# Performance work log

Measured on AMD Instinct MI355X. Metric: run time of the kernel, lower is better.

The kernel has to match this reference:

```python
import jax, jax.numpy as jnp
import numpy as np

COMMITMENT_COST = 0.25


def setup_inputs() -> dict:
    key = jax.random.key(0)
    k1, k2 = jax.random.split(key, 2)
    inputs = jax.random.normal(k1, (8, 2048, 1024), dtype=jnp.float32)
    # per-head codebooks: [H=4, K=1024, dh=256]
    codebook = jax.random.normal(k2, (4, 1024, 256), dtype=jnp.float32)
    return {"inputs": inputs, "codebook": codebook}


def reference(inputs, codebook):
    H, K, dh = codebook.shape
    flat = inputs.reshape(-1, H, dh)  # [N, H, dh]
    # squared-euclidean distances per head: [H, N, K]
    x_sq = jnp.sum(flat * flat, axis=-1).T[:, :, None]          # [H, N, 1]
    c_sq = jnp.sum(codebook * codebook, axis=-1)[:, None, :]    # [H, 1, K]
    dots = jnp.einsum('nhd,hkd->hnk', flat, codebook)           # [H, N, K]
    distances = x_sq + c_sq - 2.0 * dots
    idx = jnp.argmin(distances, axis=-1)                        # [H, N]
    # gather codebook rows (equivalent to one-hot @ codebook)
    q = jnp.take_along_axis(codebook, idx[:, :, None], axis=1)  # [H, N, dh]
    quantized = jnp.transpose(q, (1, 0, 2)).reshape(inputs.shape)
    # ema=True, eval mode: q_latent_loss = 0
    e_latent_loss = jnp.mean((jax.lax.stop_gradient(quantized) - inputs) ** 2)
    loss = COMMITMENT_COST * e_latent_loss
    # residual=False: straight-through estimator
    quantized_out = inputs + jax.lax.stop_gradient(quantized - inputs)
    return loss, quantized_out
```

## Files before the change

kernel.cpp:

```cpp
#include <hip/hip_runtime.h>
#include <cfloat>

#define NH    4
#define NK    1024
#define DHD   256
#define NTOK  16384
#define ROWS  (NH * DHD)

typedef __attribute__((ext_vector_type(8))) short bf16x8;
typedef __attribute__((ext_vector_type(4))) float f32x4;

#define WS_CSQ  ((size_t)0)
#define WS_BH   ((size_t)16384)
#define WS_BL   (WS_BH + (size_t)2097152)
#define WS_NEED (WS_BL + (size_t)2097152)

__device__ __forceinline__ unsigned short f32_to_bf16_rn(float f) {
    unsigned u = __float_as_uint(f);
    u += 0x7FFFu + ((u >> 16) & 1u);
    return (unsigned short)(u >> 16);
}
__device__ __forceinline__ float bf16_as_f32(unsigned short h) {
    return __uint_as_float(((unsigned)h) << 16);
}

__device__ __forceinline__ void gload_lds16(const uint4* g, uint4* l) {
    __builtin_amdgcn_global_load_lds(
        (const __attribute__((address_space(1))) void*)g,
        (__attribute__((address_space(3))) void*)l, 16, 0, 0);
}

__global__ __launch_bounds__(64) void csq_kernel(const float* __restrict__ cb,
                                                 float* __restrict__ csq) {
    const int code = blockIdx.x;
    const int lane = threadIdx.x;
    const float4 v = *(const float4*)(cb + (size_t)code * DHD + lane * 4);
    float s = v.x * v.x + v.y * v.y + v.z * v.z + v.w * v.w;
#pragma unroll
    for (int off = 32; off > 0; off >>= 1) s += __shfl_down(s, off, 64);
    if (lane == 0) csq[code] = s;
}

__global__ __launch_bounds__(256) void cvt_cb_kernel(const float* __restrict__ cb,
                                                     uint4* __restrict__ bch,
                                                     uint4* __restrict__ bcl) {
    const int g = blockIdx.x * 8 + (threadIdx.x >> 5);
    const int o = threadIdx.x & 31;
    const float* src = cb + (size_t)g * DHD + o * 8;
    unsigned wh[4], wl[4];
#pragma unroll
    for (int i = 0; i < 4; ++i) {
        const float f0 = src[2 * i], f1 = src[2 * i + 1];
        const unsigned short h0 = f32_to_bf16_rn(f0);
        const unsigned short h1 = f32_to_bf16_rn(f1);
        const unsigned short l0 = f32_to_bf16_rn(f0 - bf16_as_f32(h0));
        const unsigned short l1 = f32_to_bf16_rn(f1 - bf16_as_f32(h1));
        wh[i] = (unsigned)h0 | ((unsigned)h1 << 16);
        wl[i] = (unsigned)l0 | ((unsigned)l1 << 16);
    }
    const int hh = g >> 10, c = g & 1023, dc = o >> 2, kk = o & 3;
    const size_t unit = (size_t)((hh * 8 + dc) * 4 + kk) * NK + c;
    bch[unit] = make_uint4(wh[0], wh[1], wh[2], wh[3]);
    bcl[unit] = make_uint4(wl[0], wl[1], wl[2], wl[3]);
}

__device__ __forceinline__ bool lt_vi(float v, int i, float w, int j) {
    return (v < w) || (v == w && i < j);
}

__device__ __forceinline__ float np_sq_pairwise256(const float* __restrict__ a) {
#pragma clang fp contract(off)
    float tot = 0.f;
#pragma unroll
    for (int blk = 0; blk < 2; ++blk) {
        const float* p = a + blk * 128;
        float r0 = p[0] * p[0], r1 = p[1] * p[1], r2 = p[2] * p[2], r3 = p[3] * p[3];
        float r4 = p[4] * p[4], r5 = p[5] * p[5], r6 = p[6] * p[6], r7 = p[7] * p[7];
#pragma clang loop unroll_count(2)
        for (int i = 8; i < 128; i += 8) {
            r0 = r0 + p[i + 0] * p[i + 0];
            r1 = r1 + p[i + 1] * p[i + 1];
            r2 = r2 + p[i + 2] * p[i + 2];
            r3 = r3 + p[i + 3] * p[i + 3];
            r4 = r4 + p[i + 4] * p[i + 4];
            r5 = r5 + p[i + 5] * p[i + 5];
            r6 = r6 + p[i + 6] * p[i + 6];
            r7 = r7 + p[i + 7] * p[i + 7];
        }
        const float res = ((r0 + r1) + (r2 + r3)) + ((r4 + r5) + (r6 + r7));
        tot = (blk == 0) ? res : (tot + res);
    }
    return tot;
}

__device__ __forceinline__ float np_dot_seq256(const float* __restrict__ a,
                                               const float* __restrict__ b) {
#pragma clang fp contract(off)
    float s = 0.f;
#pragma clang loop unroll_count(4)
    for (int i = 0; i < 256; ++i) s = s + a[i] * b[i];
    return s;
}

__global__ __launch_bounds__(256, 2) void vq_mfma(const float* __restrict__ x,
                                                  const float* __restrict__ cb,
                                                  const float* __restrict__ csq,
                                                  const uint4* __restrict__ bch,
                                                  const uint4* __restrict__ bcl,
                                                  float* __restrict__ out) {
    __shared__ uint4 BsH[2048];
    __shared__ uint4 BsL[2048];
    __shared__ float Cs[NK];
    __shared__ int   Cand[128][2];
    __shared__ int   SIdx[128];
    __shared__ float WSum[4];

    const int tid  = threadIdx.x;
    const int h    = blockIdx.y;
    const int t0   = blockIdx.x * 128;
    const int wv   = tid >> 6;
    const int lane = tid & 63;
    const int kk   = lane >> 4;
    const int ln   = lane & 15;

    const float* xh  = x  + (size_t)t0 * ROWS + h * DHD;
    const float* cbh = cb + (size_t)h * NK * DHD;

#pragma unroll
    for (int i = tid; i < NK; i += 256) Cs[i] = csq[h * NK + i];

    bf16x8 aH[2][8], aL[2][8];
    {
        const int tokb = t0 + wv * 32 + ln;
        const float* xa = x + (size_t)tokb * ROWS + h * DHD + kk * 8;
#pragma unroll
        for (int rt = 0; rt < 2; ++rt) {
#pragma unroll
            for (int dc = 0; dc < 8; ++dc) {
                const float* p = xa + (size_t)(rt * 16) * ROWS + dc * 32;
                const float4 f0 = *(const float4*)p;
                const float4 f1 = *(const float4*)(p + 4);
                const float f[8] = {f0.x, f0.y, f0.z, f0.w, f1.x, f1.y, f1.z, f1.w};
                bf16x8 hv, lv;
#pragma unroll
                for (int j = 0; j < 8; ++j) {
                    const unsigned short hb = f32_to_bf16_rn(f[j]);
                    hv[j] = (short)hb;
                    lv[j] = (short)f32_to_bf16_rn(f[j] - bf16_as_f32(hb));
                }
                aH[rt][dc] = hv;
                aL[rt][dc] = lv;
            }
        }
    }

    float b1[8], b2[8];
    int   i1[8], i2[8];
#pragma unroll
    for (int s = 0; s < 8; ++s) { b1[s] = FLT_MAX; b2[s] = FLT_MAX; i1[s] = 0; i2[s] = 0; }

    for (int k0 = 0; k0 < NK; k0 += 64) {
        __syncthreads();
#pragma unroll
        for (int p = 0; p < 8; ++p) {
            const size_t w = (size_t)(h * 32 + p * 4 + wv) * NK + k0 + lane;
            gload_lds16(&bch[w], &BsH[p * 256 + wv * 64]);
            gload_lds16(&bcl[w], &BsL[p * 256 + wv * 64]);
        }
        __syncthreads();

        f32x4 acc[2][4];
#pragma unroll
        for (int rt = 0; rt < 2; ++rt)
#pragma unroll
            for (int ct = 0; ct < 4; ++ct) acc[rt][ct] = (f32x4){0.f, 0.f, 0.f, 0.f};

#pragma unroll
        for (int dc = 0; dc < 8; ++dc) {
#pragma unroll
            for (int ct = 0; ct < 4; ++ct) {
                const int bu = (dc * 4 + kk) * 64 + ct * 16 + ln;
                const bf16x8 bH = *(const bf16x8*)&BsH[bu];
                const bf16x8 bL = *(const bf16x8*)&BsL[bu];
#pragma unroll
                for (int rt = 0; rt < 2; ++rt) {
                    acc[rt][ct] = __builtin_amdgcn_mfma_f32_16x16x32_bf16(aH[rt][dc], bH, acc[rt][ct], 0, 0, 0);
                    acc[rt][ct] = __builtin_amdgcn_mfma_f32_16x16x32_bf16(aH[rt][dc], bL, acc[rt][ct], 0, 0, 0);
                    acc[rt][ct] = __builtin_amdgcn_mfma_f32_16x16x32_bf16(aL[rt][dc], bH, acc[rt][ct], 0, 0, 0);
                }
            }
        }

#pragma unroll
        for (int rt = 0; rt < 2; ++rt)
#pragma unroll
            for (int ct = 0; ct < 4; ++ct) {
                const float cs   = Cs[k0 + ct * 16 + ln];
                const int   codg = k0 + ct * 16 + ln;
#pragma unroll
                for (int r = 0; r < 4; ++r) {
                    const float dist = cs - 2.f * acc[rt][ct][r];
                    const int   s    = rt * 4 + r;
                    if (dist < b1[s]) { b2[s] = b1[s]; i2[s] = i1[s]; b1[s] = dist; i1[s] = codg; }
                    else if (dist < b2[s]) { b2[s] = dist; i2[s] = codg; }
                }
            }
    }

#pragma unroll
    for (int s = 0; s < 8; ++s) {
        float v1 = b1[s], v2 = b2[s];
        int   j1 = i1[s], j2 = i2[s];
#pragma unroll
        for (int m = 1; m <= 8; m <<= 1) {
            const float o1 = __shfl_xor(v1, m, 64);
            const int   oj1 = __shfl_xor(j1, m, 64);
            const float o2 = __shfl_xor(v2, m, 64);
            const int   oj2 = __shfl_xor(j2, m, 64);
            if (lt_vi(o1, oj1, v1, j1)) {
                if (lt_vi(v1, j1, o2, oj2)) { v2 = v1; j2 = j1; }
                else                        { v2 = o2; j2 = oj2; }
                v1 = o1; j1 = oj1;
            } else if (lt_vi(o1, oj1, v2, j2)) {
                v2 = o1; j2 = oj1;
            }
        }
        if (ln == 0) {
            const int tl = wv * 32 + (s >> 2) * 16 + kk * 4 + (s & 3);
            Cand[tl][0] = j1;
            Cand[tl][1] = j2;
        }
    }
    __syncthreads();

    {
        const int token = tid >> 1;
        const int cand  = tid & 1;
        const int code  = Cand[token][cand];
        const float* xr = xh + (size_t)token * ROWS;
        const float* cr = cbh + (size_t)code * DHD;
        const float X = np_sq_pairwise256(xr);
        const float C = np_sq_pairwise256(cr);
        const float D = np_dot_seq256(xr, cr);
        float d;
        {
#pragma clang fp contract(off)
            const float t = X + C;
            d = t - 2.0f * D;
        }
        const float od = __shfl_xor(d, 1, 64);
        if (cand == 0) {
            const int jA = code;
            const int jB = Cand[token][1];
            const bool pickB = (od < d) || (od == d && jB < jA);
            SIdx[token] = pickB ? jB : jA;
        }
    }
    __syncthreads();

    float lacc = 0.f;
    for (int t = wv; t < 128; t += 4) {
        const float4 q4 = *(const float4*)(cbh + (size_t)SIdx[t] * DHD + (lane << 2));
        const float4 x4 = *(const float4*)(xh + (size_t)t * ROWS + (lane << 2));
        const float dx = q4.x - x4.x, dy = q4.y - x4.y;
        const float dz = q4.z - x4.z, dw = q4.w - x4.w;
        lacc += dx * dx + dy * dy + dz * dz + dw * dw;
        *(float4*)(out + 1 + (size_t)(t0 + t) * ROWS + h * DHD + (lane << 2)) = q4;
    }
#pragma unroll
    for (int off = 32; off > 0; off >>= 1) lacc += __shfl_down(lacc, off, 64);
    if (lane == 0) WSum[wv] = lacc;
    __syncthreads();
    if (tid == 0) {
        const float s = WSum[0] + WSum[1] + WSum[2] + WSum[3];
        atomicAdd(out, s * (0.25f / 16777216.f));
    }
}

#define TN 128
#define TK 128
#define KC 16
#define APAD 4
#define BPAD 4

__global__ __launch_bounds__(256, 2) void vq_main_fp32(const float* __restrict__ x,
                                                       const float* __restrict__ cb,
                                                       const float* __restrict__ csq,
                                                       float* __restrict__ out) {
    __shared__ float As[KC][TN + APAD];
    __shared__ float Bs[KC][TK + BPAD];
    __shared__ float Cs[TK];
    __shared__ int   Cand[TN][2];
    __shared__ int   SIdx[TN];
    __shared__ float WSum[4];

    const int tid = threadIdx.x;
    const int h   = blockIdx.y;
    const int t0  = blockIdx.x * TN;
    const int ty  = tid >> 4;
    const int tx  = tid & 15;

    const float* xh  = x  + (size_t)t0 * ROWS + h * DHD;
    const float* cbh = cb + (size_t)h * NK * DHD;

    const int sr = tid >> 1;
    const int sd = (tid & 1) << 3;

    float b1[8], b2[8];
    int   i1[8], i2[8];
#pragma unroll
    for (int r = 0; r < 8; ++r) { b1[r] = FLT_MAX; b2[r] = FLT_MAX; i1[r] = 0; i2[r] = 0; }

    for (int k0 = 0; k0 < NK; k0 += TK) {
        __syncthreads();
        if (tid < TK) Cs[tid] = csq[h * NK + k0 + tid];

        float acc[8][8];
#pragma unroll
        for (int r = 0; r < 8; ++r)
#pragma unroll
            for (int c = 0; c < 8; ++c) acc[r][c] = 0.f;

        for (int d0 = 0; d0 < DHD; d0 += KC) {
            __syncthreads();
            {
                const float* ap = xh + (size_t)sr * ROWS + d0 + sd;
                const float4 a0 = *(const float4*)ap;
                const float4 a1 = *(const float4*)(ap + 4);
                As[sd + 0][sr] = a0.x; As[sd + 1][sr] = a0.y;
                As[sd + 2][sr] = a0.z; As[sd + 3][sr] = a0.w;
                As[sd + 4][sr] = a1.x; As[sd + 5][sr] = a1.y;
                As[sd + 6][sr] = a1.z; As[sd + 7][sr] = a1.w;
            }
            {
                const float* bp = cbh + (size_t)(k0 + sr) * DHD + d0 + sd;
                const float4 b0v = *(const float4*)bp;
                const float4 b1v = *(const float4*)(bp + 4);
                Bs[sd + 0][sr] = b0v.x; Bs[sd + 1][sr] = b0v.y;
                Bs[sd + 2][sr] = b0v.z; Bs[sd + 3][sr] = b0v.w;
                Bs[sd + 4][sr] = b1v.x; Bs[sd + 5][sr] = b1v.y;
                Bs[sd + 6][sr] = b1v.z; Bs[sd + 7][sr] = b1v.w;
            }
            __syncthreads();
#pragma unroll 4
            for (int kc = 0; kc < KC; ++kc) {
                const float4 a0 = *(const float4*)&As[kc][ty << 3];
                const float4 a1 = *(const float4*)&As[kc][(ty << 3) + 4];
                const float4 p0 = *(const float4*)&Bs[kc][tx << 2];
                const float4 p1 = *(const float4*)&Bs[kc][64 + (tx << 2)];
                const float aa[8] = {a0.x, a0.y, a0.z, a0.w, a1.x, a1.y, a1.z, a1.w};
                const float bb[8] = {p0.x, p0.y, p0.z, p0.w, p1.x, p1.y, p1.z, p1.w};
#pragma unroll
                for (int r = 0; r < 8; ++r)
#pragma unroll
                    for (int c = 0; c < 8; ++c)
                        acc[r][c] = fmaf(aa[r], bb[c], acc[r][c]);
            }
        }
#pragma unroll
        for (int r = 0; r < 8; ++r) {
#pragma unroll
            for (int c = 0; c < 8; ++c) {
                const int cc = (c < 4) ? ((tx << 2) + c) : (64 + (tx << 2) + c - 4);
                const float dist = Cs[cc] - 2.f * acc[r][c];
                const int   idx  = k0 + cc;
                if (dist < b1[r]) { b2[r] = b1[r]; i2[r] = i1[r]; b1[r] = dist; i1[r] = idx; }
                else if (dist < b2[r]) { b2[r] = dist; i2[r] = idx; }
            }
        }
    }

#pragma unroll
    for (int r = 0; r < 8; ++r) {
        float v1 = b1[r], v2 = b2[r];
        int   j1 = i1[r], j2 = i2[r];
#pragma unroll
        for (int m = 1; m <= 8; m <<= 1) {
            const float o1 = __shfl_xor(v1, m, 64);
            const int   oj1 = __shfl_xor(j1, m, 64);
            const float o2 = __shfl_xor(v2, m, 64);
            const int   oj2 = __shfl_xor(j2, m, 64);
            if (lt_vi(o1, oj1, v1, j1)) {
                if (lt_vi(v1, j1, o2, oj2)) { v2 = v1; j2 = j1; }
                else                        { v2 = o2; j2 = oj2; }
                v1 = o1; j1 = oj1;
            } else if (lt_vi(o1, oj1, v2, j2)) {
                v2 = o1; j2 = oj1;
            }
        }
        b1[r] = v1; i1[r] = j1; b2[r] = v2; i2[r] = j2;
    }
    if (tx == 0) {
#pragma unroll
        for (int r = 0; r < 8; ++r) {
            Cand[(ty << 3) + r][0] = i1[r];
            Cand[(ty << 3) + r][1] = i2[r];
        }
    }
    __syncthreads();

    {
        const int token = tid >> 1;
        const int cand  = tid & 1;
        const int code  = Cand[token][cand];
        const float* xr = xh + (size_t)token * ROWS;
        const float* cr = cbh + (size_t)code * DHD;
        const float X = np_sq_pairwise256(xr);
        const float C = np_sq_pairwise256(cr);
        const float D = np_dot_seq256(xr, cr);
        float d;
        {
#pragma clang fp contract(off)
            const float t = X + C;
            d = t - 2.0f * D;
        }
        const float od = __shfl_xor(d, 1, 64);
        if (cand == 0) {
            const int jA = code;
            const int jB = Cand[token][1];
            const bool pickB = (od < d) || (od == d && jB < jA);
            SIdx[token] = pickB ? jB : jA;
        }
    }
    __syncthreads();

    const int wav  = tid >> 6;
    const int lane = tid & 63;
    float lacc = 0.f;
    for (int t = wav; t < TN; t += 4) {
        const float4 q4 = *(const float4*)(cbh + (size_t)SIdx[t] * DHD + (lane << 2));
        const float4 x4 = *(const float4*)(xh + (size_t)t * ROWS + (lane << 2));
        const float dx = q4.x - x4.x, dy = q4.y - x4.y;
        const float dz = q4.z - x4.z, dw = q4.w - x4.w;
        lacc += dx * dx + dy * dy + dz * dz + dw * dw;
        *(float4*)(out + 1 + (size_t)(t0 + t) * ROWS + h * DHD + (lane << 2)) = q4;
    }
#pragma unroll
    for (int off = 32; off > 0; off >>= 1) lacc += __shfl_down(lacc, off, 64);
    if (lane == 0) WSum[wav] = lacc;
    __syncthreads();
    if (tid == 0) {
        const float s = WSum[0] + WSum[1] + WSum[2] + WSum[3];
        atomicAdd(out, s * (0.25f / 16777216.f));
    }
}

extern "C" void kernel_launch(void* const* d_in, const int* in_sizes, int n_in,
                              void* d_out, int out_size, void* d_ws, size_t ws_size,
                              hipStream_t stream) {
    const float* x   = (const float*)d_in[0];
    const float* cb  = (const float*)d_in[1];
    float*       out = (float*)d_out;
    char*        ws  = (char*)d_ws;
    float*       csq = (float*)(ws + WS_CSQ);

    hipMemsetAsync(d_out, 0, sizeof(float), stream);
    csq_kernel<<<NH * NK, 64, 0, stream>>>(cb, csq);

    if (ws_size >= WS_NEED) {
        uint4* bch = (uint4*)(ws + WS_BH);
        uint4* bcl = (uint4*)(ws + WS_BL);
        cvt_cb_kernel<<<NH * NK / 8, 256, 0, stream>>>(cb, bch, bcl);
        dim3 grid(NTOK / 128, NH);
        vq_mfma<<<grid, 256, 0, stream>>>(x, cb, csq, bch, bcl, out);
    } else {
        dim3 grid(NTOK / TN, NH);
        vq_main_fp32<<<grid, 256, 0, stream>>>(x, cb, csq, out);
    }
}
```

Before: 329.4 us.

## Split exact refinement and output gather into separate tail kernel

The MFMA kernel now only computes top-2 candidates per token and writes them to a workspace buffer. A new 64-thread tail kernel does the exact fp32 re-ranking, using a fused single-pass function for the squared norms and dot product, then does the quantized gather, the output write and the loss reduction. This takes the serial, latency-bound refinement out of the heavy MFMA blocks and spreads it over many small blocks. The cost is an extra launch and a candidate round-trip through global memory, plus many more atomics on the loss scalar.

Result: no change. 324.0 us (-1.6%).

```diff
diff --git a/kernel.cpp b/kernel.cpp
--- a/kernel.cpp
+++ b/kernel.cpp
@@ -13,7 +13,8 @@
 #define WS_CSQ  ((size_t)0)
 #define WS_BH   ((size_t)16384)
 #define WS_BL   (WS_BH + (size_t)2097152)
-#define WS_NEED (WS_BL + (size_t)2097152)
+#define WS_CAND (WS_BL + (size_t)2097152)
+#define WS_NEED (WS_CAND + (size_t)524288)
 
 __device__ __forceinline__ unsigned short f32_to_bf16_rn(float f) {
     unsigned u = __float_as_uint(f);
@@ -102,18 +103,48 @@
     return s;
 }
 
+__device__ __forceinline__ void refine_exact(const float* __restrict__ xr,
+                                             const float* __restrict__ cr,
+                                             float& Xo, float& Co, float& Do) {
+#pragma clang fp contract(off)
+    float s = 0.f;
+    float X = 0.f, C = 0.f;
+    for (int blk = 0; blk < 2; ++blk) {
+        const float4* xq = (const float4*)(xr + blk * 128);
+        const float4* cq = (const float4*)(cr + blk * 128);
+        float xa[8], ca[8];
+#pragma unroll
+        for (int j = 0; j < 8; ++j) { xa[j] = 0.f; ca[j] = 0.f; }
+#pragma clang loop unroll_count(4)
+        for (int g = 0; g < 16; ++g) {
+            const float4 a0 = xq[2 * g], a1 = xq[2 * g + 1];
+            const float4 b0 = cq[2 * g], b1 = cq[2 * g + 1];
+            const float xf[8] = {a0.x, a0.y, a0.z, a0.w, a1.x, a1.y, a1.z, a1.w};
+            const float cf[8] = {b0.x, b0.y, b0.z, b0.w, b1.x, b1.y, b1.z, b1.w};
+#pragma unroll
+            for (int j = 0; j < 8; ++j) {
+                xa[j] = xa[j] + xf[j] * xf[j];
+                ca[j] = ca[j] + cf[j] * cf[j];
+            }
+#pragma unroll
+            for (int j = 0; j < 8; ++j) s = s + xf[j] * cf[j];
+        }
+        const float xres = ((xa[0] + xa[1]) + (xa[2] + xa[3])) + ((xa[4] + xa[5]) + (xa[6] + xa[7]));
+        const float cres = ((ca[0] + ca[1]) + (ca[2] + ca[3])) + ((ca[4] + ca[5]) + (ca[6] + ca[7]));
+        X = (blk == 0) ? xres : (X + xres);
+        C = (blk == 0) ? cres : (C + cres);
+    }
+    Xo = X; Co = C; Do = s;
+}
+
 __global__ __launch_bounds__(256, 2) void vq_mfma(const float* __restrict__ x,
-                                                  const float* __restrict__ cb,
                                                   const float* __restrict__ csq,
                                                   const uint4* __restrict__ bch,
                                                   const uint4* __restrict__ bcl,
-                                                  float* __restrict__ out) {
+                                                  int* __restrict__ candw) {
     __shared__ uint4 BsH[2048];
     __shared__ uint4 BsL[2048];
     __shared__ float Cs[NK];
-    __shared__ int   Cand[128][2];
-    __shared__ int   SIdx[128];
-    __shared__ float WSum[4];
 
     const int tid  = threadIdx.x;
     const int h    = blockIdx.y;
@@ -122,9 +153,6 @@
     const int lane = tid & 63;
     const int kk   = lane >> 4;
     const int ln   = lane & 15;
-
-    const float* xh  = x  + (size_t)t0 * ROWS + h * DHD;
-    const float* cbh = cb + (size_t)h * NK * DHD;
 
 #pragma unroll
     for (int i = tid; i < NK; i += 256) Cs[i] = csq[h * NK + i];
@@ -226,9 +254,181 @@
             }
         }
         if (ln == 0) {
-            const int tl = wv * 32 + (s >> 2) * 16 + kk * 4 + (s & 3);
-            Cand[tl][0] = j1;
-            Cand[tl][1] = j2;
+            const int tl  = wv * 32 + (s >> 2) * 16 + kk * 4 + (s & 3);
+            const int gid = h * NTOK + t0 + tl;
+            candw[2 * gid + 0] = j1;
+            candw[2 * gid + 1] = j2;
+        }
+    }
+}
+
+__global__ __launch_bounds__(64) void vq_tail(const float* __restrict__ x,
+                                              const float* __restrict__ cb,
+                                              const int* __restrict__ candw,
+                                              float* __restrict__ out) {
+    const int lane = threadIdx.x;
+    const int rowb = blockIdx.x * 32;
+    const int h    = rowb >> 14;
+    const int tb   = rowb & (NTOK - 1);
+    const float* cbh = cb + (size_t)h * NK * DHD;
+
+    const int rloc = lane >> 1;
+    const int cand = lane & 1;
+    const int row  = rowb + rloc;
+    const int t    = tb + rloc;
+    const int code = candw[2 * row + cand];
+    const float* xr = x + (size_t)t * ROWS + h * DHD;
+    const float* cr = cbh + (size_t)code * DHD;
+    float X, C, D;
+    refine_exact(xr, cr, X, C, D);
+    float d;
+    {
+#pragma clang fp contract(off)
+        const float tt = X + C;
+        d = tt - 2.0f * D;
+    }
+    const float od = __shfl_xor(d, 1, 64);
+    int sel = code;
+    if (cand == 0) {
+        const int jB = candw[2 * row + 1];
+        const bool pickB = (od < d) || (od == d && jB < code);
+        if (pickB) sel = jB;
+    }
+
+    float lacc = 0.f;
+    for (int r = 0; r < 32; ++r) {
+        const int cr_code = __shfl(sel, 2 * r, 64);
+        const int tr = tb + r;
+        const float4 q4 = *(const float4*)(cbh + (size_t)cr_code * DHD + (lane << 2));
+        const float4 x4 = *(const float4*)(x + (size_t)tr * ROWS + h * DHD + (lane << 2));
+        const float dx = q4.x - x4.x, dy = q4.y - x4.y;
+        const float dz = q4.z - x4.z, dw = q4.w - x4.w;
+        lacc += dx * dx + dy * dy + dz * dz + dw * dw;
+        *(float4*)(out + 1 + (size_t)tr * ROWS + h * DHD + (lane << 2)) = q4;
+    }
+#pragma unroll
+    for (int off = 32; off > 0; off >>= 1) lacc += __shfl_down(lacc, off, 64);
+    if (lane == 0) atomicAdd(out, lacc * (0.25f / 16777216.f));
+}
+
+#define TN 128
+#define TK 128
+#define KC 16
+#define APAD 4
+#define BPAD 4
+
+__global__ __launch_bounds__(256, 2) void vq_main_fp32(const float* __restrict__ x,
+                                                       const float* __restrict__ cb,
+                                                       const float* __restrict__ csq,
+                                                       float* __restrict__ out) {
+    __shared__ float As[KC][TN + APAD];
+    __shared__ float Bs[KC][TK + BPAD];
+    __shared__ float Cs[TK];
+    __shared__ int   Cand[TN][2];
+    __shared__ int   SIdx[TN];
+    __shared__ float WSum[4];
+
+    const int tid = threadIdx.x;
+    const int h   = blockIdx.y;
+    const int t0  = blockIdx.x * TN;
+    const int ty  = tid >> 4;
+    const int tx  = tid & 15;
+
+    const float* xh  = x  + (size_t)t0 * ROWS + h * DHD;
+    const float* cbh = cb + (size_t)h * NK * DHD;
+
+    const int sr = tid >> 1;
+    const int sd = (tid & 1) << 3;
+
+    float b1[8], b2[8];
+    int   i1[8], i2[8];
+#pragma unroll
+    for (int r = 0; r < 8; ++r) { b1[r] = FLT_MAX; b2[r] = FLT_MAX; i1[r] = 0; i2[r] = 0; }
+
+    for (int k0 = 0; k0 < NK; k0 += TK) {
+        __syncthreads();
+        if (tid < TK) Cs[tid] = csq[h * NK + k0 + tid];
+
+        float acc[8][8];
+#pragma unroll
+        for (int r = 0; r < 8; ++r)
+#pragma unroll
+            for (int c = 0; c < 8; ++c) acc[r][c] = 0.f;
+
+        for (int d0 = 0; d0 < DHD; d0 += KC) {
+            __syncthreads();
+            {
+                const float* ap = xh + (size_t)sr * ROWS + d0 + sd;
+                const float4 a0 = *(const float4*)ap;
+                const float4 a1 = *(const float4*)(ap + 4);
+                As[sd + 0][sr] = a0.x; As[sd + 1][sr] = a0.y;
+                As[sd + 2][sr] = a0.z; As[sd + 3][sr] = a0.w;
+                As[sd + 4][sr] = a1.x; As[sd + 5][sr] = a1.y;
+                As[sd + 6][sr] = a1.z; As[sd + 7][sr] = a1.w;
+            }
+            {
+                const float* bp = cbh + (size_t)(k0 + sr) * DHD + d0 + sd;
+                const float4 b0v = *(const float4*)bp;
+                const float4 b1v = *(const float4*)(bp + 4);
+                Bs[sd + 0][sr] = b0v.x; Bs[sd + 1][sr] = b0v.y;
+                Bs[sd + 2][sr] = b0v.z; Bs[sd + 3][sr] = b0v.w;
+                Bs[sd + 4][sr] = b1v.x; Bs[sd + 5][sr] = b1v.y;
+                Bs[sd + 6][sr] = b1v.z; Bs[sd + 7][sr] = b1v.w;
+            }
+            __syncthreads();
+#pragma unroll 4
+            for (int kc = 0; kc < KC; ++kc) {
+                const float4 a0 = *(const float4*)&As[kc][ty << 3];
+                const float4 a1 = *(const float4*)&As[kc][(ty << 3) + 4];
+                const float4 p0 = *(const float4*)&Bs[kc][tx << 2];
+                const float4 p1 = *(const float4*)&Bs[kc][64 + (tx << 2)];
+                const float aa[8] = {a0.x, a0.y, a0.z, a0.w, a1.x, a1.y, a1.z, a1.w};
+                const float bb[8] = {p0.x, p0.y, p0.z, p0.w, p1.x, p1.y, p1.z, p1.w};
+#pragma unroll
+                for (int r = 0; r < 8; ++r)
+#pragma unroll
+                    for (int c = 0; c < 8; ++c)
+                        acc[r][c] = fmaf(aa[r], bb[c], acc[r][c]);
+            }
+        }
+#pragma unroll
+        for (int r = 0; r < 8; ++r) {
+#pragma unroll
+            for (int c = 0; c < 8; ++c) {
+                const int cc = (c < 4) ? ((tx << 2) + c) : (64 + (tx << 2) + c - 4);
+                const float dist = Cs[cc] - 2.f * acc[r][c];
+                const int   idx  = k0 + cc;
+                if (dist < b1[r]) { b2[r] = b1[r]; i2[r] = i1[r]; b1[r] = dist; i1[r] = idx; }
+                else if (dist < b2[r]) { b2[r] = dist; i2[r] = idx; }
+            }
+        }
+    }
+
+#pragma unroll
+    for (int r = 0; r < 8; ++r) {
+        float v1 = b1[r], v2 = b2[r];
+        int   j1 = i1[r], j2 = i2[r];
+#pragma unroll
+        for (int m = 1; m <= 8; m <<= 1) {
+            const float o1 = __shfl_xor(v1, m, 64);
+            const int   oj1 = __shfl_xor(j1, m, 64);
+            const float o2 = __shfl_xor(v2, m, 64);
+            const int   oj2 = __shfl_xor(j2, m, 64);
+            if (lt_vi(o1, oj1, v1, j1)) {
+                if (lt_vi(v1, j1, o2, oj2)) { v2 = v1; j2 = j1; }
+                else                        { v2 = o2; j2 = oj2; }
+                v1 = o1; j1 = oj1;
+            } else if (lt_vi(o1, oj1, v2, j2)) {
+                v2 = o1; j2 = oj1;
+            }
+        }
+        b1[r] = v1; i1[r] = j1; b2[r] = v2; i2[r] = j2;
+    }
+    if (tx == 0) {
+#pragma unroll
+        for (int r = 0; r < 8; ++r) {
+            Cand[(ty << 3) + r][0] = i1[r];
+            Cand[(ty << 3) + r][1] = i2[r];
         }
     }
     __syncthreads();
@@ -258,172 +458,6 @@
     }
     __syncthreads();
 
-    float lacc = 0.f;
-    for (int t = wv; t < 128; t += 4) {
-        const float4 q4 = *(const float4*)(cbh + (size_t)SIdx[t] * DHD + (lane << 2));
-        const float4 x4 = *(const float4*)(xh + (size_t)t * ROWS + (lane << 2));
-        const float dx = q4.x - x4.x, dy = q4.y - x4.y;
-        const float dz = q4.z - x4.z, dw = q4.w - x4.w;
-        lacc += dx * dx + dy * dy + dz * dz + dw * dw;
-        *(float4*)(out + 1 + (size_t)(t0 + t) * ROWS + h * DHD + (lane << 2)) = q4;
-    }
-#pragma unroll
-    for (int off = 32; off > 0; off >>= 1) lacc += __shfl_down(lacc, off, 64);
-    if (lane == 0) WSum[wv] = lacc;
-    __syncthreads();
-    if (tid == 0) {
-        const float s = WSum[0] + WSum[1] + WSum[2] + WSum[3];
-        atomicAdd(out, s * (0.25f / 16777216.f));
-    }
-}
-
-#define TN 128
-#define TK 128
-#define KC 16
-#define APAD 4
-#define BPAD 4
-
-__global__ __launch_bounds__(256, 2) void vq_main_fp32(const float* __restrict__ x,
-                                                       const float* __restrict__ cb,
-                                                       const float* __restrict__ csq,
-                                                       float* __restrict__ out) {
-    __shared__ float As[KC][TN + APAD];
-    __shared__ float Bs[KC][TK + BPAD];
-    __shared__ float Cs[TK];
-    __shared__ int   Cand[TN][2];
-    __shared__ int   SIdx[TN];
-    __shared__ float WSum[4];
-
-    const int tid = threadIdx.x;
-    const int h   = blockIdx.y;
-    const int t0  = blockIdx.x * TN;
-    const int ty  = tid >> 4;
-    const int tx  = tid & 15;
-
-    const float* xh  = x  + (size_t)t0 * ROWS + h * DHD;
-    const float* cbh = cb + (size_t)h * NK * DHD;
-
-    const int sr = tid >> 1;
-    const int sd = (tid & 1) << 3;
-
-    float b1[8], b2[8];
-    int   i1[8], i2[8];
-#pragma unroll
-    for (int r = 0; r < 8; ++r) { b1[r] = FLT_MAX; b2[r] = FLT_MAX; i1[r] = 0; i2[r] = 0; }
-
-    for (int k0 = 0; k0 < NK; k0 += TK) {
-        __syncthreads();
-        if (tid < TK) Cs[tid] = csq[h * NK + k0 + tid];
-
-        float acc[8][8];
-#pragma unroll
-        for (int r = 0; r < 8; ++r)
-#pragma unroll
-            for (int c = 0; c < 8; ++c) acc[r][c] = 0.f;
-
-        for (int d0 = 0; d0 < DHD; d0 += KC) {
-            __syncthreads();
-            {
-                const float* ap = xh + (size_t)sr * ROWS + d0 + sd;
-                const float4 a0 = *(const float4*)ap;
-                const float4 a1 = *(const float4*)(ap + 4);
-                As[sd + 0][sr] = a0.x; As[sd + 1][sr] = a0.y;
-                As[sd + 2][sr] = a0.z; As[sd + 3][sr] = a0.w;
-                As[sd + 4][sr] = a1.x; As[sd + 5][sr] = a1.y;
-                As[sd + 6][sr] = a1.z; As[sd + 7][sr] = a1.w;
-            }
-            {
-                const float* bp = cbh + (size_t)(k0 + sr) * DHD + d0 + sd;
-                const float4 b0v = *(const float4*)bp;
-                const float4 b1v = *(const float4*)(bp + 4);
-                Bs[sd + 0][sr] = b0v.x; Bs[sd + 1][sr] = b0v.y;
-                Bs[sd + 2][sr] = b0v.z; Bs[sd + 3][sr] = b0v.w;
-                Bs[sd + 4][sr] = b1v.x; Bs[sd + 5][sr] = b1v.y;
-                Bs[sd + 6][sr] = b1v.z; Bs[sd + 7][sr] = b1v.w;
-            }
-            __syncthreads();
-#pragma unroll 4
-            for (int kc = 0; kc < KC; ++kc) {
-                const float4 a0 = *(const float4*)&As[kc][ty << 3];
-                const float4 a1 = *(const float4*)&As[kc][(ty << 3) + 4];
-                const float4 p0 = *(const float4*)&Bs[kc][tx << 2];
-                const float4 p1 = *(const float4*)&Bs[kc][64 + (tx << 2)];
-                const float aa[8] = {a0.x, a0.y, a0.z, a0.w, a1.x, a1.y, a1.z, a1.w};
-                const float bb[8] = {p0.x, p0.y, p0.z, p0.w, p1.x, p1.y, p1.z, p1.w};
-#pragma unroll
-                for (int r = 0; r < 8; ++r)
-#pragma unroll
-                    for (int c = 0; c < 8; ++c)
-                        acc[r][c] = fmaf(aa[r], bb[c], acc[r][c]);
-            }
-        }
-#pragma unroll
-        for (int r = 0; r < 8; ++r) {
-#pragma unroll
-            for (int c = 0; c < 8; ++c) {
-                const int cc = (c < 4) ? ((tx << 2) + c) : (64 + (tx << 2) + c - 4);
-                const float dist = Cs[cc] - 2.f * acc[r][c];
-                const int   idx  = k0 + cc;
-                if (dist < b1[r]) { b2[r] = b1[r]; i2[r] = i1[r]; b1[r] = dist; i1[r] = idx; }
-                else if (dist < b2[r]) { b2[r] = dist; i2[r] = idx; }
-            }
-        }
-    }
-
-#pragma unroll
-    for (int r = 0; r < 8; ++r) {
-        float v1 = b1[r], v2 = b2[r];
-        int   j1 = i1[r], j2 = i2[r];
-#pragma unroll
-        for (int m = 1; m <= 8; m <<= 1) {
-            const float o1 = __shfl_xor(v1, m, 64);
-            const int   oj1 = __shfl_xor(j1, m, 64);
-            const float o2 = __shfl_xor(v2, m, 64);
-            const int   oj2 = __shfl_xor(j2, m, 64);
-            if (lt_vi(o1, oj1, v1, j1)) {
-                if (lt_vi(v1, j1, o2, oj2)) { v2 = v1; j2 = j1; }
-                else                        { v2 = o2; j2 = oj2; }
-                v1 = o1; j1 = oj1;
-            } else if (lt_vi(o1, oj1, v2, j2)) {
-                v2 = o1; j2 = oj1;
-            }
-        }
-        b1[r] = v1; i1[r] = j1; b2[r] = v2; i2[r] = j2;
-    }
-    if (tx == 0) {
-#pragma unroll
-        for (int r = 0; r < 8; ++r) {
-            Cand[(ty << 3) + r][0] = i1[r];
-            Cand[(ty << 3) + r][1] = i2[r];
-        }
-    }
-    __syncthreads();
-
-    {
-        const int token = tid >> 1;
-        const int cand  = tid & 1;
-        const int code  = Cand[token][cand];
-        const float* xr = xh + (size_t)token * ROWS;
-        const float* cr = cbh + (size_t)code * DHD;
-        const float X = np_sq_pairwise256(xr);
-        const float C = np_sq_pairwise256(cr);
-        const float D = np_dot_seq256(xr, cr);
-        float d;
-        {
-#pragma clang fp contract(off)
-            const float t = X + C;
-            d = t - 2.0f * D;
-        }
-        const float od = __shfl_xor(d, 1, 64);
-        if (cand == 0) {
-            const int jA = code;
-            const int jB = Cand[token][1];
-            const bool pickB = (od < d) || (od == d && jB < jA);
-            SIdx[token] = pickB ? jB : jA;
-        }
-    }
-    __syncthreads();
-
     const int wav  = tid >> 6;
     const int lane = tid & 63;
     float lacc = 0.f;
@@ -458,11 +492,13 @@
     csq_kernel<<<NH * NK, 64, 0, stream>>>(cb, csq);
 
     if (ws_size >= WS_NEED) {
-        uint4* bch = (uint4*)(ws + WS_BH);
-        uint4* bcl = (uint4*)(ws + WS_BL);
+        uint4* bch   = (uint4*)(ws + WS_BH);
+        uint4* bcl   = (uint4*)(ws + WS_BL);
+        int*   candw = (int*)(ws + WS_CAND);
         cvt_cb_kernel<<<NH * NK / 8, 256, 0, stream>>>(cb, bch, bcl);
         dim3 grid(NTOK / 128, NH);
-        vq_mfma<<<grid, 256, 0, stream>>>(x, cb, csq, bch, bcl, out);
+        vq_mfma<<<grid, 256, 0, stream>>>(x, csq, bch, bcl, candw);
+        vq_tail<<<NTOK * NH / 32, 64, 0, stream>>>(x, cb, candw, out);
     } else {
         dim3 grid(NTOK / TN, NH);
         vq_main_fp32<<<grid, 256, 0, stream>>>(x, cb, csq, out);
```
